# Kernel tuning notes

Hardware: AMD Instinct MI355X
Metric: run time of the kernel (lower is better)

Reference implementation:

```python
import jax, jax.numpy as jnp
import numpy as np

NHEAD = 8
GROUPS = 32   # GroupNorm(32) assumed for ConvNormActivation's norm (diffusion-UNet convention)
EPS = 1e-5


def group_norm(x, scale, bias):
    # x: [B, C, H, W]
    b, c, h, w = x.shape
    xg = x.reshape(b, GROUPS, c // GROUPS, h, w)
    mu = xg.mean(axis=(2, 3, 4), keepdims=True)
    var = xg.var(axis=(2, 3, 4), keepdims=True)
    xg = (xg - mu) * jax.lax.rsqrt(var + EPS)
    return xg.reshape(b, c, h, w) * scale[None, :, None, None] + bias[None, :, None, None]


def setup_inputs() -> dict:
    key = jax.random.key(0)
    ks = jax.random.split(key, 3)
    B, C, H, W = 8, 512, 32, 32
    s = 0.02
    return {
        "x": jax.random.normal(ks[0], (B, C, H, W), jnp.float32),
        "gn1_scale": jnp.ones((C,), jnp.float32),
        "gn1_bias": jnp.zeros((C,), jnp.float32),
        "w_qkv": jax.random.normal(ks[1], (3 * C, C), jnp.float32) * s,  # 1x1 conv kernel
        "b_qkv": jnp.zeros((3 * C,), jnp.float32),
        "w_proj": jax.random.normal(ks[2], (C, C), jnp.float32) * s,    # 1x1 conv kernel
        "b_proj": jnp.zeros((C,), jnp.float32),
        "gn2_scale": jnp.ones((C,), jnp.float32),
        "gn2_bias": jnp.zeros((C,), jnp.float32),
    }


def reference(x, gn1_scale, gn1_bias, w_qkv, b_qkv, w_proj, b_proj, gn2_scale, gn2_bias):
    b, c, h, w = x.shape
    n = h * w
    ch = c // NHEAD

    # qkv = Conv1x1(GroupNorm(x))  (norm_first=True)
    hn = group_norm(x, gn1_scale, gn1_bias)
    qkv = jnp.einsum('bchw,oc->bohw', hn, w_qkv) + b_qkv[None, :, None, None]

    # [B, 3C, H, W] -> [B*heads, 3*ch, N], split into q,k,v (matches torch reshape/split)
    qkv = qkv.reshape(b * NHEAD, 3 * ch, n)
    q, k, v = jnp.split(qkv, 3, axis=1)

    scale = ch ** -0.25
    wgt = jnp.einsum('bct,bcs->bts', q * scale, k * scale)   # [B*H, N, N]
    wgt = jax.nn.softmax(wgt, axis=-1)                        # stable (max-subtract fused)
    a = jnp.einsum('bts,bcs->bct', wgt, v).reshape(b, c, h, w)

    # proj_out = GroupNorm(Conv1x1(a))  (norm after conv, Identity activation)
    out = jnp.einsum('bchw,oc->bohw', a, w_proj) + b_proj[None, :, None, None]
    out = group_norm(out, gn2_scale, gn2_bias)
    return x + out
```

## Files before the change

### kernel.cpp

```cpp
#include <hip/hip_runtime.h>
#include <math.h>

#define NB 8
#define NC 512
#define NHW 1024
#define NG 32
#define CPG 16
#define QKV_C 1536
#define EPS 1e-5f
#define QSCALE 0.18033688011112042f

typedef float  f32x4  __attribute__((ext_vector_type(4)));
typedef __bf16 bf16x8 __attribute__((ext_vector_type(8)));
typedef __bf16 bf16x4 __attribute__((ext_vector_type(4)));

__device__ __forceinline__ void gload_lds16(const void* g, void* l) {
    __builtin_amdgcn_global_load_lds(
        (const __attribute__((address_space(1))) void*)g,
        (__attribute__((address_space(3))) void*)l, 16, 0, 0);
}

__device__ __forceinline__ void dma_drain() {
    asm volatile("s_waitcnt vmcnt(0)" ::: "memory");
}

__global__ __launch_bounds__(256) void gn_stats_k(const float* __restrict__ x,
                                                  float* __restrict__ mu,
                                                  float* __restrict__ rinv) {
    const int grp = blockIdx.x;
    const float4* p4 = (const float4*)(x + (size_t)grp * (CPG * NHW));
    float s = 0.f, s2 = 0.f;
    for (int i = threadIdx.x; i < CPG * NHW / 4; i += 256) {
        float4 v = p4[i];
        s  += v.x + v.y + v.z + v.w;
        s2 += v.x * v.x + v.y * v.y + v.z * v.z + v.w * v.w;
    }
    for (int off = 32; off > 0; off >>= 1) {
        s  += __shfl_down(s, off);
        s2 += __shfl_down(s2, off);
    }
    __shared__ float ls[4], ls2[4];
    const int wv = threadIdx.x >> 6;
    if ((threadIdx.x & 63) == 0) { ls[wv] = s; ls2[wv] = s2; }
    __syncthreads();
    if (threadIdx.x == 0) {
        float S  = ls[0] + ls[1] + ls[2] + ls[3];
        float S2 = ls2[0] + ls2[1] + ls2[2] + ls2[3];
        const float inv = 1.f / (float)(CPG * NHW);
        float m = S * inv;
        float var = S2 * inv - m * m;
        mu[grp]   = m;
        rinv[grp] = rsqrtf(var + EPS);
    }
}

__global__ __launch_bounds__(256) void gn_apply_t_k(const float* __restrict__ x,
                                                    const float* __restrict__ mu,
                                                    const float* __restrict__ rinv,
                                                    const float* __restrict__ sc,
                                                    const float* __restrict__ bi,
                                                    __bf16* __restrict__ hnT) {
    __shared__ float T[64][65];
    const int tid = threadIdx.x;
    const int nb = blockIdx.x * 64, cb = blockIdx.y * 64, b = blockIdx.z;
    const int col = (tid & 15) * 4;
    const int rb = tid >> 4;
    #pragma unroll
    for (int rr = 0; rr < 4; rr++) {
        int cl = rr * 16 + rb;
        int c = cb + cl;
        int grp = b * NG + (c >> 4);
        float a = sc[c] * rinv[grp];
        float d = bi[c] - mu[grp] * a;
        float4 v4 = *(const float4*)&x[((size_t)(b * NC + c)) * NHW + nb + col];
        T[cl][col + 0] = v4.x * a + d;
        T[cl][col + 1] = v4.y * a + d;
        T[cl][col + 2] = v4.z * a + d;
        T[cl][col + 3] = v4.w * a + d;
    }
    __syncthreads();
    const int nl = tid >> 2;
    const int c0 = (tid & 3) * 16;
    bf16x8 o0, o1;
    #pragma unroll
    for (int i = 0; i < 8; i++) o0[i] = (__bf16)T[c0 + i][nl];
    #pragma unroll
    for (int i = 0; i < 8; i++) o1[i] = (__bf16)T[c0 + 8 + i][nl];
    __bf16* dst = hnT + ((size_t)(b * NHW + nb + nl)) * NC + cb + c0;
    *(bf16x8*)dst = o0;
    *(bf16x8*)(dst + 8) = o1;
}

__global__ __launch_bounds__(256) void cvt2_k(const float* __restrict__ s1,
                                              __bf16* __restrict__ d1,
                                              const float* __restrict__ s2,
                                              __bf16* __restrict__ d2,
                                              int n1_4) {
    const int i = blockIdx.x * 256 + threadIdx.x;
    const float4* s = (i < n1_4) ? (const float4*)s1 + i : (const float4*)s2 + (i - n1_4);
    bf16x4* d = (i < n1_4) ? (bf16x4*)d1 + i : (bf16x4*)d2 + (i - n1_4);
    float4 v = *s;
    bf16x4 o;
    o[0] = (__bf16)v.x; o[1] = (__bf16)v.y; o[2] = (__bf16)v.z; o[3] = (__bf16)v.w;
    *d = o;
}

__device__ __forceinline__ void mm_stage(const __bf16* __restrict__ W,
                                         const __bf16* __restrict__ Bm,
                                         int K, int m0, int n0, int k0,
                                         __bf16* As, __bf16* Bs) {
    const int tid = threadIdx.x;
    const int w = tid >> 6, lane = tid & 63;
    const int lr = lane >> 2, lk = (lane & 3) * 8;
    #pragma unroll
    for (int i = 0; i < 2; i++) {
        int rb = (w * 2 + i) * 16;
        gload_lds16(W  + (size_t)(m0 + rb + lr) * K + k0 + lk, As + rb * 32);
        gload_lds16(Bm + (size_t)(n0 + rb + lr) * K + k0 + lk, Bs + rb * 32);
    }
}

__device__ __forceinline__ void mm_core(const __bf16* __restrict__ W,
                                        const __bf16* __restrict__ Bm,
                                        int K, int m0, int n0,
                                        __bf16* As, __bf16* Bs,
                                        f32x4 (&acc)[4][4]) {
    const int tid = threadIdx.x;
    const int w = tid >> 6, lane = tid & 63;
    const int l15 = lane & 15, quad = lane >> 4;
    const int wm = (w & 1) * 64, wn = (w >> 1) * 64;
    const int nk = K >> 5;
    mm_stage(W, Bm, K, m0, n0, 0, As, Bs);
    for (int it = 0; it < nk; it++) {
        const int cur = (it & 1) * 4096;
        dma_drain();
        __syncthreads();
        if (it + 1 < nk)
            mm_stage(W, Bm, K, m0, n0, (it + 1) * 32, As + (4096 - cur), Bs + (4096 - cur));
        bf16x8 af[4], bfv[4];
        #pragma unroll
        for (int mi = 0; mi < 4; mi++)
            af[mi] = *(const bf16x8*)(As + cur + (wm + mi * 16 + l15) * 32 + quad * 8);
        #pragma unroll
        for (int ni = 0; ni < 4; ni++)
            bfv[ni] = *(const bf16x8*)(Bs + cur + (wn + ni * 16 + l15) * 32 + quad * 8);
        #pragma unroll
        for (int mi = 0; mi < 4; mi++)
            #pragma unroll
            for (int ni = 0; ni < 4; ni++)
                acc[mi][ni] = __builtin_amdgcn_mfma_f32_16x16x32_bf16(
                    af[mi], bfv[ni], acc[mi][ni], 0, 0, 0);
    }
}

__global__ __launch_bounds__(256) void qkv_gemm_k(const __bf16* __restrict__ W,
                                                  const __bf16* __restrict__ hnT,
                                                  const float* __restrict__ bias,
                                                  __bf16* __restrict__ qT,
                                                  __bf16* __restrict__ kT,
                                                  __bf16* __restrict__ v) {
    __shared__ __bf16 As[2 * 128 * 32];
    __shared__ __bf16 Bs[2 * 128 * 32];
    const int m0 = blockIdx.x * 128, n0 = blockIdx.y * 128, b = blockIdx.z;
    f32x4 acc[4][4] = {};
    mm_core(W, hnT + (size_t)b * NHW * NC, NC, m0, n0, As, Bs, acc);
    const int tid = threadIdx.x;
    const int w = tid >> 6, lane = tid & 63;
    const int l15 = lane & 15, quad = lane >> 4;
    const int wm = (w & 1) * 64, wn = (w >> 1) * 64;
    #pragma unroll
    for (int mi = 0; mi < 4; mi++) {
        #pragma unroll
        for (int r = 0; r < 4; r++) {
            int m = m0 + wm + mi * 16 + quad * 4 + r;
            float bb = bias[m];
            int h = m / 192;
            int rr = m - h * 192;
            int bh = b * 8 + h;
            #pragma unroll
            for (int ni = 0; ni < 4; ni++) {
                int n = n0 + wn + ni * 16 + l15;
                float val = acc[mi][ni][r] + bb;
                if (rr < 64) {
                    qT[((size_t)bh << 16) + n * 64 + rr] = (__bf16)(val * QSCALE);
                } else if (rr < 128) {
                    kT[((size_t)bh << 16) + n * 64 + (rr - 64)] = (__bf16)val;
                } else {
                    v[((size_t)(bh * 64 + rr - 128)) * NHW + n] = (__bf16)val;
                }
            }
        }
    }
}

__global__ __launch_bounds__(256) void proj_gemm_k(const __bf16* __restrict__ W,
                                                   const __bf16* __restrict__ aT,
                                                   const float* __restrict__ bias,
                                                   float* __restrict__ proj) {
    __shared__ __bf16 As[2 * 128 * 32];
    __shared__ __bf16 Bs[2 * 128 * 32];
    const int m0 = blockIdx.x * 128, n0 = blockIdx.y * 128, b = blockIdx.z;
    f32x4 acc[4][4] = {};
    mm_core(W, aT + (size_t)b * NHW * NC, NC, m0, n0, As, Bs, acc);
    const int tid = threadIdx.x;
    const int w = tid >> 6, lane = tid & 63;
    const int l15 = lane & 15, quad = lane >> 4;
    const int wm = (w & 1) * 64, wn = (w >> 1) * 64;
    #pragma unroll
    for (int mi = 0; mi < 4; mi++) {
        #pragma unroll
        for (int r = 0; r < 4; r++) {
            int m = m0 + wm + mi * 16 + quad * 4 + r;
            float bb = bias[m];
            #pragma unroll
            for (int ni = 0; ni < 4; ni++) {
                int n = n0 + wn + ni * 16 + l15;
                proj[((size_t)(b * NC + m)) * NHW + n] = acc[mi][ni][r] + bb;
            }
        }
    }
}

__global__ __launch_bounds__(256) void attn_k(const __bf16* __restrict__ qT,
                                              const __bf16* __restrict__ kT,
                                              const __bf16* __restrict__ vv,
                                              __bf16* __restrict__ aT) {
    __shared__ __bf16 Qt[2 * 64 * 32];
    __shared__ __bf16 Kt[2 * 2 * 64 * 32];
    __shared__ __bf16 Vt[2 * 2 * 64 * 32];
    __shared__ __bf16 Ps[64 * 72];
    const int tid = threadIdx.x;
    const int w = tid >> 6, lane = tid & 63;
    const int l15 = lane & 15, quad = lane >> 4;
    const int lr = lane >> 2, lk = (lane & 3) * 8;
    const int bh = blockIdx.x, t0 = blockIdx.y * 64;
    const __bf16* qb = qT + ((size_t)bh << 16);
    const __bf16* kb = kT + ((size_t)bh << 16);
    const __bf16* vb = vv + ((size_t)bh << 6) * NHW;

    #pragma unroll
    for (int i = 0; i < 2; i++) {
        int inst = w * 2 + i;
        int ch = inst >> 2, tb = (inst & 3) * 16;
        gload_lds16(qb + (size_t)(t0 + tb + lr) * 64 + ch * 32 + lk,
                    Qt + ch * 2048 + tb * 32);
    }
    {
        const int s0 = 0;
        #pragma unroll
        for (int i = 0; i < 4; i++) {
            int inst = w * 4 + i;
            if (inst < 8) {
                int ch = inst >> 2, sb = (inst & 3) * 16;
                gload_lds16(kb + (size_t)(s0 + sb + lr) * 64 + ch * 32 + lk,
                            Kt + ch * 2048 + sb * 32);
            } else {
                int i2 = inst - 8;
                int ch = i2 >> 2, cb = (i2 & 3) * 16;
                gload_lds16(vb + (size_t)(cb + lr) * NHW + s0 + ch * 32 + lk,
                            Vt + ch * 2048 + cb * 32);
            }
        }
    }
    float lpart[4] = {};
    f32x4 Oacc[4] = {};

    for (int it = 0; it < 16; it++) {
        const int cur = (it & 1) * 4096;
        const int nxt = 4096 - cur;
        dma_drain();
        __syncthreads();
        if (it + 1 < 16) {
            const int s0 = (it + 1) * 64;
            #pragma unroll
            for (int i = 0; i < 4; i++) {
                int inst = w * 4 + i;
                if (inst < 8) {
                    int ch = inst >> 2, sb = (inst & 3) * 16;
                    gload_lds16(kb + (size_t)(s0 + sb + lr) * 64 + ch * 32 + lk,
                                Kt + nxt + ch * 2048 + sb * 32);
                } else {
                    int i2 = inst - 8;
                    int ch = i2 >> 2, cb = (i2 & 3) * 16;
                    gload_lds16(vb + (size_t)(cb + lr) * NHW + s0 + ch * 32 + lk,
                                Vt + nxt + ch * 2048 + cb * 32);
                }
            }
        }
        f32x4 sacc[4] = {};
        #pragma unroll
        for (int ch = 0; ch < 2; ch++) {
            bf16x8 a = *(const bf16x8*)(Qt + ch * 2048 + (w * 16 + l15) * 32 + quad * 8);
            #pragma unroll
            for (int j = 0; j < 4; j++) {
                bf16x8 bfr = *(const bf16x8*)(Kt + cur + ch * 2048 + (j * 16 + l15) * 32 + quad * 8);
                sacc[j] = __builtin_amdgcn_mfma_f32_16x16x32_bf16(a, bfr, sacc[j], 0, 0, 0);
            }
        }
        #pragma unroll
        for (int r = 0; r < 4; r++) {
            int t = w * 16 + quad * 4 + r;
            #pragma unroll
            for (int j = 0; j < 4; j++) {
                float p = __builtin_amdgcn_exp2f(sacc[j][r]);
                lpart[r] += p;
                Ps[t * 72 + j * 16 + l15] = (__bf16)p;
            }
        }
        #pragma unroll
        for (int ch = 0; ch < 2; ch++) {
            bf16x8 a = *(const bf16x8*)(Ps + (w * 16 + l15) * 72 + ch * 32 + quad * 8);
            #pragma unroll
            for (int ci = 0; ci < 4; ci++) {
                bf16x8 bfr = *(const bf16x8*)(Vt + cur + ch * 2048 + (ci * 16 + l15) * 32 + quad * 8);
                Oacc[ci] = __builtin_amdgcn_mfma_f32_16x16x32_bf16(a, bfr, Oacc[ci], 0, 0, 0);
            }
        }
    }
    const int b = bh >> 3, hh = bh & 7;
    #pragma unroll
    for (int r = 0; r < 4; r++) {
        float sum = lpart[r];
        sum += __shfl_xor(sum, 1);
        sum += __shfl_xor(sum, 2);
        sum += __shfl_xor(sum, 4);
        sum += __shfl_xor(sum, 8);
        float inv = 1.f / sum;
        int t = w * 16 + quad * 4 + r;
        size_t base = ((size_t)(b * NHW + t0 + t)) * NC + hh * 64;
        #pragma unroll
        for (int ci = 0; ci < 4; ci++)
            aT[base + ci * 16 + l15] = (__bf16)(Oacc[ci][r] * inv);
    }
}

__global__ __launch_bounds__(256) void final_k(const float* __restrict__ x,
                                               const float* __restrict__ p,
                                               const float* __restrict__ mu,
                                               const float* __restrict__ rinv,
                                               const float* __restrict__ sc,
                                               const float* __restrict__ bi,
                                               float* __restrict__ out) {
    const int i4 = blockIdx.x * 256 + threadIdx.x;
    const int c  = (i4 >> 8) & (NC - 1);
    const int b  = i4 >> 17;
    const int grp = b * NG + (c >> 4);
    const float m = mu[grp], r = rinv[grp];
    const float a = sc[c] * r;
    const float d = bi[c] - m * a;
    float4 xv = ((const float4*)x)[i4];
    float4 pv = ((const float4*)p)[i4];
    float4 o = make_float4(xv.x + pv.x * a + d, xv.y + pv.y * a + d,
                           xv.z + pv.z * a + d, xv.w + pv.w * a + d);
    ((float4*)out)[i4] = o;
}

extern "C" void kernel_launch(void* const* d_in, const int* in_sizes, int n_in,
                              void* d_out, int out_size, void* d_ws, size_t ws_size,
                              hipStream_t stream) {
    const float* x      = (const float*)d_in[0];
    const float* gn1_s  = (const float*)d_in[1];
    const float* gn1_b  = (const float*)d_in[2];
    const float* w_qkv  = (const float*)d_in[3];
    const float* b_qkv  = (const float*)d_in[4];
    const float* w_proj = (const float*)d_in[5];
    const float* b_proj = (const float*)d_in[6];
    const float* gn2_s  = (const float*)d_in[7];
    const float* gn2_b  = (const float*)d_in[8];
    float* out = (float*)d_out;

    char* p = (char*)d_ws;
    __bf16* hnT  = (__bf16*)p;            p += (size_t)8 * 1024 * 512 * 2;
    __bf16* qT   = (__bf16*)p;            p += (size_t)64 * 1024 * 64 * 2;
    __bf16* kT   = (__bf16*)p;            p += (size_t)64 * 1024 * 64 * 2;
    __bf16* vB   = (__bf16*)p;            p += (size_t)64 * 64 * 1024 * 2;
    __bf16* aT   = (__bf16*)p;            p += (size_t)8 * 1024 * 512 * 2;
    float*  proj = (float*)p;             p += (size_t)8 * 512 * 1024 * 4;
    __bf16* wq   = (__bf16*)p;            p += (size_t)QKV_C * NC * 2;
    __bf16* wp   = (__bf16*)p;            p += (size_t)NC * NC * 2;
    float*  mu1  = (float*)p;             p += 256 * 4;
    float*  ri1  = (float*)p;             p += 256 * 4;
    float*  mu2  = (float*)p;             p += 256 * 4;
    float*  ri2  = (float*)p;             p += 256 * 4;

    gn_stats_k<<<256, 256, 0, stream>>>(x, mu1, ri1);
    cvt2_k<<<(QKV_C * NC + NC * NC) / 1024, 256, 0, stream>>>(
        w_qkv, wq, w_proj, wp, QKV_C * NC / 4);
    gn_apply_t_k<<<dim3(16, 8, 8), 256, 0, stream>>>(x, mu1, ri1, gn1_s, gn1_b, hnT);

    qkv_gemm_k<<<dim3(12, 8, 8), 256, 0, stream>>>(wq, hnT, b_qkv, qT, kT, vB);

    attn_k<<<dim3(64, 16), 256, 0, stream>>>(qT, kT, vB, aT);

    proj_gemm_k<<<dim3(4, 8, 8), 256, 0, stream>>>(wp, aT, b_proj, proj);

    gn_stats_k<<<256, 256, 0, stream>>>(proj, mu2, ri2);
    final_k<<<4096, 256, 0, stream>>>(x, proj, mu2, ri2, gn2_s, gn2_b, out);
}
```

Baseline: 195.7 us.

## Fuse prep kernels, register-resident attention P, and fold GN2 stats into proj GEMM

```diff
diff --git a/kernel.cpp b/kernel.cpp
--- a/kernel.cpp
+++ b/kernel.cpp
@@ -13,6 +13,7 @@
 typedef float  f32x4  __attribute__((ext_vector_type(4)));
 typedef __bf16 bf16x8 __attribute__((ext_vector_type(8)));
 typedef __bf16 bf16x4 __attribute__((ext_vector_type(4)));
+typedef short  s16x4  __attribute__((ext_vector_type(4)));
 
 __device__ __forceinline__ void gload_lds16(const void* g, void* l) {
     __builtin_amdgcn_global_load_lds(
@@ -24,33 +25,67 @@
     asm volatile("s_waitcnt vmcnt(0)" ::: "memory");
 }
 
-__global__ __launch_bounds__(256) void gn_stats_k(const float* __restrict__ x,
-                                                  float* __restrict__ mu,
-                                                  float* __restrict__ rinv) {
-    const int grp = blockIdx.x;
-    const float4* p4 = (const float4*)(x + (size_t)grp * (CPG * NHW));
-    float s = 0.f, s2 = 0.f;
-    for (int i = threadIdx.x; i < CPG * NHW / 4; i += 256) {
-        float4 v = p4[i];
-        s  += v.x + v.y + v.z + v.w;
-        s2 += v.x * v.x + v.y * v.y + v.z * v.z + v.w * v.w;
-    }
-    for (int off = 32; off > 0; off >>= 1) {
-        s  += __shfl_down(s, off);
-        s2 += __shfl_down(s2, off);
-    }
-    __shared__ float ls[4], ls2[4];
-    const int wv = threadIdx.x >> 6;
-    if ((threadIdx.x & 63) == 0) { ls[wv] = s; ls2[wv] = s2; }
-    __syncthreads();
-    if (threadIdx.x == 0) {
-        float S  = ls[0] + ls[1] + ls[2] + ls[3];
-        float S2 = ls2[0] + ls2[1] + ls2[2] + ls2[3];
-        const float inv = 1.f / (float)(CPG * NHW);
-        float m = S * inv;
-        float var = S2 * inv - m * m;
-        mu[grp]   = m;
-        rinv[grp] = rsqrtf(var + EPS);
+__device__ __forceinline__ f32x4 mfma16(bf16x4 a, bf16x4 b, f32x4 c) {
+#if __has_builtin(__builtin_amdgcn_mfma_f32_16x16x16bf16_1k)
+    return __builtin_amdgcn_mfma_f32_16x16x16bf16_1k(
+        __builtin_bit_cast(s16x4, a), __builtin_bit_cast(s16x4, b), c, 0, 0, 0);
+#else
+    f32x4 d;
+    asm volatile("v_mfma_f32_16x16x16_bf16 %0, %1, %2, %3"
+                 : "=v"(d) : "v"(a), "v"(b), "v"(c));
+    return d;
+#endif
+}
+
+__global__ __launch_bounds__(256) void prep_k(const float* __restrict__ x,
+                                              float* __restrict__ mu,
+                                              float* __restrict__ rinv,
+                                              const float* __restrict__ w1,
+                                              __bf16* __restrict__ d1,
+                                              const float* __restrict__ w2,
+                                              __bf16* __restrict__ d2,
+                                              float* __restrict__ gstat) {
+    const int bi = blockIdx.x;
+    if (bi < 256) {
+        const int grp = bi;
+        const float4* p4 = (const float4*)(x + (size_t)grp * (CPG * NHW));
+        float s = 0.f, s2 = 0.f;
+        for (int i = threadIdx.x; i < CPG * NHW / 4; i += 256) {
+            float4 v = p4[i];
+            s  += v.x + v.y + v.z + v.w;
+            s2 += v.x * v.x + v.y * v.y + v.z * v.z + v.w * v.w;
+        }
+        for (int off = 32; off > 0; off >>= 1) {
+            s  += __shfl_down(s, off);
+            s2 += __shfl_down(s2, off);
+        }
+        __shared__ float ls[4], ls2[4];
+        const int wv = threadIdx.x >> 6;
+        if ((threadIdx.x & 63) == 0) { ls[wv] = s; ls2[wv] = s2; }
+        __syncthreads();
+        if (threadIdx.x == 0) {
+            float S = ls[0] + ls[1] + ls[2] + ls[3];
+            float S2 = ls2[0] + ls2[1] + ls2[2] + ls2[3];
+            const float inv = 1.f / (float)(CPG * NHW);
+            float m = S * inv;
+            float var = S2 * inv - m * m;
+            mu[grp] = m;
+            rinv[grp] = rsqrtf(var + EPS);
+        }
+        if (bi == 0 && threadIdx.x < 256) {
+            gstat[threadIdx.x] = 0.f;
+            gstat[threadIdx.x + 256] = 0.f;
+        }
+    } else {
+        const int n1_4 = QKV_C * NC / 4;
+        const int i = (bi - 256) * 256 + threadIdx.x;
+        const float4* s = (i < n1_4) ? (const float4*)w1 + i
+                                     : (const float4*)w2 + (i - n1_4);
+        bf16x4* d = (i < n1_4) ? (bf16x4*)d1 + i : (bf16x4*)d2 + (i - n1_4);
+        float4 v = *s;
+        bf16x4 o;
+        o[0] = (__bf16)v.x; o[1] = (__bf16)v.y; o[2] = (__bf16)v.z; o[3] = (__bf16)v.w;
+        *d = o;
     }
 }
 
@@ -89,20 +124,6 @@
     __bf16* dst = hnT + ((size_t)(b * NHW + nb + nl)) * NC + cb + c0;
     *(bf16x8*)dst = o0;
     *(bf16x8*)(dst + 8) = o1;
-}
-
-__global__ __launch_bounds__(256) void cvt2_k(const float* __restrict__ s1,
-                                              __bf16* __restrict__ d1,
-                                              const float* __restrict__ s2,
-                                              __bf16* __restrict__ d2,
-                                              int n1_4) {
-    const int i = blockIdx.x * 256 + threadIdx.x;
-    const float4* s = (i < n1_4) ? (const float4*)s1 + i : (const float4*)s2 + (i - n1_4);
-    bf16x4* d = (i < n1_4) ? (bf16x4*)d1 + i : (bf16x4*)d2 + (i - n1_4);
-    float4 v = *s;
-    bf16x4 o;
-    o[0] = (__bf16)v.x; o[1] = (__bf16)v.y; o[2] = (__bf16)v.z; o[3] = (__bf16)v.w;
-    *d = o;
 }
 
 __device__ __forceinline__ void mm_stage(const __bf16* __restrict__ W,
@@ -196,7 +217,8 @@
 __global__ __launch_bounds__(256) void proj_gemm_k(const __bf16* __restrict__ W,
                                                    const __bf16* __restrict__ aT,
                                                    const float* __restrict__ bias,
-                                                   float* __restrict__ proj) {
+                                                   __bf16* __restrict__ projb,
+                                                   float* __restrict__ gstat) {
     __shared__ __bf16 As[2 * 128 * 32];
     __shared__ __bf16 Bs[2 * 128 * 32];
     const int m0 = blockIdx.x * 128, n0 = blockIdx.y * 128, b = blockIdx.z;
@@ -206,6 +228,7 @@
     const int w = tid >> 6, lane = tid & 63;
     const int l15 = lane & 15, quad = lane >> 4;
     const int wm = (w & 1) * 64, wn = (w >> 1) * 64;
+    float bsum[4] = {}, bsq[4] = {};
     #pragma unroll
     for (int mi = 0; mi < 4; mi++) {
         #pragma unroll
@@ -215,8 +238,25 @@
             #pragma unroll
             for (int ni = 0; ni < 4; ni++) {
                 int n = n0 + wn + ni * 16 + l15;
-                proj[((size_t)(b * NC + m)) * NHW + n] = acc[mi][ni][r] + bb;
-            }
+                float val = acc[mi][ni][r] + bb;
+                projb[((size_t)(b * NC + m)) * NHW + n] = (__bf16)val;
+                bsum[mi] += val;
+                bsq[mi] += val * val;
+            }
+        }
+    }
+    #pragma unroll
+    for (int mi = 0; mi < 4; mi++) {
+        float s = bsum[mi], q = bsq[mi];
+        #pragma unroll
+        for (int off = 1; off < 64; off <<= 1) {
+            s += __shfl_xor(s, off);
+            q += __shfl_xor(q, off);
+        }
+        if (lane == 0) {
+            int grp = b * NG + ((m0 + wm) >> 4) + mi;
+            atomicAdd(&gstat[grp], s);
+            atomicAdd(&gstat[256 + grp], q);
         }
     }
 }
@@ -225,45 +265,40 @@
                                               const __bf16* __restrict__ kT,
                                               const __bf16* __restrict__ vv,
                                               __bf16* __restrict__ aT) {
-    __shared__ __bf16 Qt[2 * 64 * 32];
-    __shared__ __bf16 Kt[2 * 2 * 64 * 32];
-    __shared__ __bf16 Vt[2 * 2 * 64 * 32];
-    __shared__ __bf16 Ps[64 * 72];
+    __shared__ __bf16 Kt[2 * 4096];
+    __shared__ __bf16 Vt[2 * 4096];
     const int tid = threadIdx.x;
     const int w = tid >> 6, lane = tid & 63;
     const int l15 = lane & 15, quad = lane >> 4;
     const int lr = lane >> 2, lk = (lane & 3) * 8;
-    const int bh = blockIdx.x, t0 = blockIdx.y * 64;
+    const int bh = blockIdx.x, t0 = blockIdx.y * 128;
     const __bf16* qb = qT + ((size_t)bh << 16);
     const __bf16* kb = kT + ((size_t)bh << 16);
     const __bf16* vb = vv + ((size_t)bh << 6) * NHW;
 
-    #pragma unroll
-    for (int i = 0; i < 2; i++) {
-        int inst = w * 2 + i;
-        int ch = inst >> 2, tb = (inst & 3) * 16;
-        gload_lds16(qb + (size_t)(t0 + tb + lr) * 64 + ch * 32 + lk,
-                    Qt + ch * 2048 + tb * 32);
-    }
-    {
-        const int s0 = 0;
-        #pragma unroll
-        for (int i = 0; i < 4; i++) {
-            int inst = w * 4 + i;
-            if (inst < 8) {
-                int ch = inst >> 2, sb = (inst & 3) * 16;
-                gload_lds16(kb + (size_t)(s0 + sb + lr) * 64 + ch * 32 + lk,
-                            Kt + ch * 2048 + sb * 32);
-            } else {
-                int i2 = inst - 8;
-                int ch = i2 >> 2, cb = (i2 & 3) * 16;
-                gload_lds16(vb + (size_t)(cb + lr) * NHW + s0 + ch * 32 + lk,
-                            Vt + ch * 2048 + cb * 32);
-            }
-        }
-    }
-    float lpart[4] = {};
-    f32x4 Oacc[4] = {};
+    bf16x8 qfr[2][2];
+    #pragma unroll
+    for (int tb = 0; tb < 2; tb++)
+        #pragma unroll
+        for (int ch = 0; ch < 2; ch++)
+            qfr[tb][ch] = *(const bf16x8*)(qb + (size_t)(t0 + w * 32 + tb * 16 + l15) * 64
+                                           + ch * 32 + quad * 8);
+    #pragma unroll
+    for (int i = 0; i < 4; i++) {
+        int inst = w * 4 + i;
+        if (inst < 8) {
+            int ch = inst >> 2, sb = (inst & 3) * 16;
+            gload_lds16(kb + (size_t)(sb + lr) * 64 + ch * 32 + lk,
+                        Kt + ch * 2048 + sb * 32);
+        } else {
+            int i2 = inst - 8;
+            int ch = i2 >> 2, cb = (i2 & 3) * 16;
+            gload_lds16(vb + (size_t)(cb + lr) * NHW + ch * 32 + lk,
+                        Vt + ch * 2048 + cb * 32);
+        }
+    }
+    float lp[2] = {0.f, 0.f};
+    f32x4 Oacc[2][4] = {};
 
     for (int it = 0; it < 16; it++) {
         const int cur = (it & 1) * 4096;
@@ -287,57 +322,65 @@
                 }
             }
         }
-        f32x4 sacc[4] = {};
-        #pragma unroll
-        for (int ch = 0; ch < 2; ch++) {
-            bf16x8 a = *(const bf16x8*)(Qt + ch * 2048 + (w * 16 + l15) * 32 + quad * 8);
+        f32x4 sacc[2][4] = {};
+        #pragma unroll
+        for (int ch = 0; ch < 2; ch++)
             #pragma unroll
             for (int j = 0; j < 4; j++) {
-                bf16x8 bfr = *(const bf16x8*)(Kt + cur + ch * 2048 + (j * 16 + l15) * 32 + quad * 8);
-                sacc[j] = __builtin_amdgcn_mfma_f32_16x16x32_bf16(a, bfr, sacc[j], 0, 0, 0);
-            }
-        }
+                bf16x8 kfr = *(const bf16x8*)(Kt + cur + ch * 2048
+                                              + (j * 16 + l15) * 32 + quad * 8);
+                sacc[0][j] = __builtin_amdgcn_mfma_f32_16x16x32_bf16(
+                    kfr, qfr[0][ch], sacc[0][j], 0, 0, 0);
+                sacc[1][j] = __builtin_amdgcn_mfma_f32_16x16x32_bf16(
+                    kfr, qfr[1][ch], sacc[1][j], 0, 0, 0);
+            }
+        bf16x4 pf[2][4];
+        #pragma unroll
+        for (int tb = 0; tb < 2; tb++)
+            #pragma unroll
+            for (int j = 0; j < 4; j++) {
+                bf16x4 pk;
+                #pragma unroll
+                for (int r = 0; r < 4; r++) {
+                    float pv = __builtin_amdgcn_exp2f(sacc[tb][j][r]);
+                    lp[tb] += pv;
+                    pk[r] = (__bf16)pv;
+                }
+                pf[tb][j] = pk;
+            }
+        #pragma unroll
+        for (int jt = 0; jt < 4; jt++) {
+            int sg = jt * 16 + quad * 4;
+            const __bf16* vbase = Vt + cur + (sg >> 5) * 2048 + (sg & 31);
+            #pragma unroll
+            for (int ci = 0; ci < 4; ci++) {
+                bf16x4 vfr = *(const bf16x4*)(vbase + (ci * 16 + l15) * 32);
+                Oacc[0][ci] = mfma16(pf[0][jt], vfr, Oacc[0][ci]);
+                Oacc[1][ci] = mfma16(pf[1][jt], vfr, Oacc[1][ci]);
+            }
+        }
+    }
+    const int b = bh >> 3, hh = bh & 7;
+    #pragma unroll
+    for (int tb = 0; tb < 2; tb++) {
+        float s = lp[tb];
+        s += __shfl_xor(s, 16);
+        s += __shfl_xor(s, 32);
         #pragma unroll
         for (int r = 0; r < 4; r++) {
-            int t = w * 16 + quad * 4 + r;
-            #pragma unroll
-            for (int j = 0; j < 4; j++) {
-                float p = __builtin_amdgcn_exp2f(sacc[j][r]);
-                lpart[r] += p;
-                Ps[t * 72 + j * 16 + l15] = (__bf16)p;
-            }
-        }
-        #pragma unroll
-        for (int ch = 0; ch < 2; ch++) {
-            bf16x8 a = *(const bf16x8*)(Ps + (w * 16 + l15) * 72 + ch * 32 + quad * 8);
-            #pragma unroll
-            for (int ci = 0; ci < 4; ci++) {
-                bf16x8 bfr = *(const bf16x8*)(Vt + cur + ch * 2048 + (ci * 16 + l15) * 32 + quad * 8);
-                Oacc[ci] = __builtin_amdgcn_mfma_f32_16x16x32_bf16(a, bfr, Oacc[ci], 0, 0, 0);
-            }
-        }
-    }
-    const int b = bh >> 3, hh = bh & 7;
-    #pragma unroll
-    for (int r = 0; r < 4; r++) {
-        float sum = lpart[r];
-        sum += __shfl_xor(sum, 1);
-        sum += __shfl_xor(sum, 2);
-        sum += __shfl_xor(sum, 4);
-        sum += __shfl_xor(sum, 8);
-        float inv = 1.f / sum;
-        int t = w * 16 + quad * 4 + r;
-        size_t base = ((size_t)(b * NHW + t0 + t)) * NC + hh * 64;
-        #pragma unroll
-        for (int ci = 0; ci < 4; ci++)
-            aT[base + ci * 16 + l15] = (__bf16)(Oacc[ci][r] * inv);
+            float inv = 1.f / __shfl(s, quad * 4 + r);
+            int t = t0 + w * 32 + tb * 16 + quad * 4 + r;
+            size_t base = ((size_t)(b * NHW + t)) * NC + hh * 64;
+            #pragma unroll
+            for (int ci = 0; ci < 4; ci++)
+                aT[base + ci * 16 + l15] = (__bf16)(Oacc[tb][ci][r] * inv);
+        }
     }
 }
 
 __global__ __launch_bounds__(256) void final_k(const float* __restrict__ x,
-                                               const float* __restrict__ p,
-                                               const float* __restrict__ mu,
-                                               const float* __restrict__ rinv,
+                                               const __bf16* __restrict__ pb,
+                                               const float* __restrict__ gstat,
                                                const float* __restrict__ sc,
                                                const float* __restrict__ bi,
                                                float* __restrict__ out) {
@@ -345,13 +388,16 @@
     const int c  = (i4 >> 8) & (NC - 1);
     const int b  = i4 >> 17;
     const int grp = b * NG + (c >> 4);
-    const float m = mu[grp], r = rinv[grp];
+    const float inv = 1.f / (float)(CPG * NHW);
+    const float m = gstat[grp] * inv;
+    const float var = gstat[256 + grp] * inv - m * m;
+    const float r = rsqrtf(var + EPS);
     const float a = sc[c] * r;
     const float d = bi[c] - m * a;
     float4 xv = ((const float4*)x)[i4];
-    float4 pv = ((const float4*)p)[i4];
-    float4 o = make_float4(xv.x + pv.x * a + d, xv.y + pv.y * a + d,
-                           xv.z + pv.z * a + d, xv.w + pv.w * a + d);
+    bf16x4 pv = ((const bf16x4*)pb)[i4];
+    float4 o = make_float4(xv.x + (float)pv[0] * a + d, xv.y + (float)pv[1] * a + d,
+                           xv.z + (float)pv[2] * a + d, xv.w + (float)pv[3] * a + d);
     ((float4*)out)[i4] = o;
 }
 
@@ -370,30 +416,26 @@
     float* out = (float*)d_out;
 
     char* p = (char*)d_ws;
-    __bf16* hnT  = (__bf16*)p;            p += (size_t)8 * 1024 * 512 * 2;
-    __bf16* qT   = (__bf16*)p;            p += (size_t)64 * 1024 * 64 * 2;
-    __bf16* kT   = (__bf16*)p;            p += (size_t)64 * 1024 * 64 * 2;
-    __bf16* vB   = (__bf16*)p;            p += (size_t)64 * 64 * 1024 * 2;
-    __bf16* aT   = (__bf16*)p;            p += (size_t)8 * 1024 * 512 * 2;
-    float*  proj = (float*)p;             p += (size_t)8 * 512 * 1024 * 4;
-    __bf16* wq   = (__bf16*)p;            p += (size_t)QKV_C * NC * 2;
-    __bf16* wp   = (__bf16*)p;            p += (size_t)NC * NC * 2;
-    float*  mu1  = (float*)p;             p += 256 * 4;
-    float*  ri1  = (float*)p;             p += 256 * 4;
-    float*  mu2  = (float*)p;             p += 256 * 4;
-    float*  ri2  = (float*)p;             p += 256 * 4;
-
-    gn_stats_k<<<256, 256, 0, stream>>>(x, mu1, ri1);
-    cvt2_k<<<(QKV_C * NC + NC * NC) / 1024, 256, 0, stream>>>(
-        w_qkv, wq, w_proj, wp, QKV_C * NC / 4);
+    __bf16* hnT   = (__bf16*)p;           p += (size_t)8 * 1024 * 512 * 2;
+    __bf16* qT    = (__bf16*)p;           p += (size_t)64 * 1024 * 64 * 2;
+    __bf16* kT    = (__bf16*)p;           p += (size_t)64 * 1024 * 64 * 2;
+    __bf16* vB    = (__bf16*)p;           p += (size_t)64 * 64 * 1024 * 2;
+    __bf16* aT    = (__bf16*)p;           p += (size_t)8 * 1024 * 512 * 2;
+    __bf16* projb = (__bf16*)p;           p += (size_t)8 * 512 * 1024 * 2;
+    __bf16* wq    = (__bf16*)p;           p += (size_t)QKV_C * NC * 2;
+    __bf16* wp    = (__bf16*)p;           p += (size_t)NC * NC * 2;
+    float*  mu1   = (float*)p;            p += 256 * 4;
+    float*  ri1   = (float*)p;            p += 256 * 4;
+    float*  gstat = (float*)p;            p += 512 * 4;
+
+    prep_k<<<1280, 256, 0, stream>>>(x, mu1, ri1, w_qkv, wq, w_proj, wp, gstat);
     gn_apply_t_k<<<dim3(16, 8, 8), 256, 0, stream>>>(x, mu1, ri1, gn1_s, gn1_b, hnT);
 
     qkv_gemm_k<<<dim3(12, 8, 8), 256, 0, stream>>>(wq, hnT, b_qkv, qT, kT, vB);
 
-    attn_k<<<dim3(64, 16), 256, 0, stream>>>(qT, kT, vB, aT);
-
-    proj_gemm_k<<<dim3(4, 8, 8), 256, 0, stream>>>(wp, aT, b_proj, proj);
-
-    gn_stats_k<<<256, 256, 0, stream>>>(proj, mu2, ri2);
-    final_k<<<4096, 256, 0, stream>>>(x, proj, mu2, ri2, gn2_s, gn2_b, out);
-}
+    attn_k<<<dim3(64, 8), 256, 0, stream>>>(qT, kT, vB, aT);
+
+    proj_gemm_k<<<dim3(4, 8, 8), 256, 0, stream>>>(wp, aT, b_proj, projb, gstat);
+
+    final_k<<<4096, 256, 0, stream>>>(x, projb, gstat, gn2_s, gn2_b, out);
+}
```

Result: no change. 193.5 us (-1.1%).
